# Kernel tuning notes

Measured on AMD Instinct MI355X. Metric: run time of the kernel, lower is better.

Reference implementation:

```python
import jax, jax.numpy as jnp
import numpy as np

SIGMA = 0.2
BN_EPS = 1e-5


def setup_inputs() -> dict:
    key = jax.random.key(0)
    k1, k2, k3, k4 = jax.random.split(key, 4)
    B, N, K = 8, 16384, 64
    normals = jax.random.normal(k1, (B, 3, N), dtype=jnp.float32)
    # normalize to unit normals (faithful to what the module consumes in practice)
    normals = normals / jnp.linalg.norm(normals, axis=1, keepdims=True)
    neighbor_idx = jax.random.randint(k2, (B, N, 3), 0, N, dtype=jnp.int64)
    weight_alpha = jax.random.uniform(k3, (1, K, 4), dtype=jnp.float32) * np.pi
    weight_beta = jax.random.uniform(k4, (1, K, 4), dtype=jnp.float32) * (2 * np.pi)
    bn_gamma = jnp.ones((K,), dtype=jnp.float32)
    bn_beta = jnp.zeros((K,), dtype=jnp.float32)
    return {
        "normals": normals,
        "neighbor_idx": neighbor_idx,
        "weight_alpha": weight_alpha,
        "weight_beta": weight_beta,
        "bn_gamma": bn_gamma,
        "bn_beta": bn_beta,
    }


def reference(normals, neighbor_idx, weight_alpha, weight_beta, bn_gamma, bn_beta):
    # normals: (B, 3, N); neighbor_idx: (B, N, 3)
    # kernel directions on unit sphere: W[c, k, m], c in xyz, m in 4 points per kernel
    W = jnp.concatenate(
        [
            jnp.sin(weight_alpha) * jnp.cos(weight_beta),
            jnp.sin(weight_alpha) * jnp.sin(weight_beta),
            jnp.cos(weight_alpha),
        ],
        axis=0,
    )  # (3, K, 4)

    # gather neighbor normals: nbr[b, c, i, j] = normals[b, c, neighbor_idx[b, i, j]]
    nbr = jax.vmap(lambda nm, idx: nm[:, idx])(normals, neighbor_idx)  # (B, 3, N, 3)
    F = jnp.concatenate([normals[:, :, :, None], nbr], axis=3)  # (B, 3, N, 4) face points p

    # squared distances via ||f||^2 + ||w||^2 - 2 f.w  (avoids 6D broadcast of torch code)
    dots = jnp.einsum("bcnp,ckm->bknpm", F, W)  # (B, K, N, 4, 4)
    F2 = jnp.sum(F * F, axis=1)[:, None, :, :, None]  # (B, 1, N, 4, 1)
    W2 = jnp.sum(W * W, axis=0)[None, :, None, None, :]  # (1, K, 1, 1, 4)
    dist = F2 + W2 - 2.0 * dots  # (B, K, N, 4, 4)

    inv = -1.0 / (2.0 * SIGMA * SIGMA)
    feat = jnp.sum(jnp.exp(dist * inv), axis=(3, 4)) / 16.0  # (B, K, N)

    # BatchNorm1d (training mode, biased variance over batch+spatial dims) + ReLU
    mean = jnp.mean(feat, axis=(0, 2), keepdims=True)
    var = jnp.var(feat, axis=(0, 2), keepdims=True)
    xhat = (feat - mean) * jax.lax.rsqrt(var + BN_EPS)
    out = bn_gamma[None, :, None] * xhat + bn_beta[None, :, None]
    return jax.nn.relu(out)
```

## Files before the change

### kernel.cpp

```cpp
#include <hip/hip_runtime.h>

#define BB 8
#define NN 16384
#define KK 64

#if __has_builtin(__builtin_amdgcn_exp2f)
#define EXP2(x) __builtin_amdgcn_exp2f(x)
#else
#define EXP2(x) exp2f(x)
#endif

#define LOG2E 1.44269504088896340736f
#define CW (25.0f * LOG2E)
#define CE (-12.5f * LOG2E)

__global__ __launch_bounds__(256) void fkc_main(
    const float* __restrict__ normals,
    const int*   __restrict__ nidx,
    const float* __restrict__ walpha,
    const float* __restrict__ wbeta,
    float* __restrict__ out)
{
    __shared__ float4 WV[KK * 4];

    const int tid = threadIdx.x;

    {
        float a = walpha[tid];
        float b = wbeta[tid];
        float sa = __sinf(a);
        WV[tid] = make_float4(CW * sa * __cosf(b),
                              CW * sa * __sinf(b),
                              CW * __cosf(a), 0.0f);
    }
    __syncthreads();

    const int pg = blockIdx.x >> 1;
    const int k0 = (blockIdx.x & 1) * 32;
    const int gid = pg * 256 + tid;
    const int b = gid >> 14;
    const int n = gid & (NN - 1);
    const float* nb = normals + b * 3 * NN;

    float fx[4], fy[4], fz[4], e2[4];
    fx[0] = nb[n];
    fy[0] = nb[NN + n];
    fz[0] = nb[2 * NN + n];
    const int ibase = (b * NN + n) * 3;
#pragma unroll
    for (int j = 0; j < 3; ++j) {
        int id = nidx[ibase + j];
        fx[j + 1] = nb[id];
        fy[j + 1] = nb[NN + id];
        fz[j + 1] = nb[2 * NN + id];
    }
#pragma unroll
    for (int p = 0; p < 4; ++p) {
        float n2 = fmaf(fx[p], fx[p], fmaf(fy[p], fy[p], fz[p] * fz[p]));
        e2[p] = CE * (n2 + 1.0f);
    }

    float* orow = out + (b * KK + k0) * NN + n;
#pragma unroll 2
    for (int k = 0; k < 32; ++k) {
        float acc = 0.0f;
#pragma unroll
        for (int m = 0; m < 4; ++m) {
            float4 w = WV[((k0 + k) << 2) + m];
#pragma unroll
            for (int p = 0; p < 4; ++p) {
                float arg = fmaf(fz[p], w.z,
                            fmaf(fy[p], w.y,
                            fmaf(fx[p], w.x, e2[p])));
                acc += EXP2(arg);
            }
        }
        orow[k * NN] = acc;
    }
}

__global__ __launch_bounds__(256) void fkc_reduce(
    const float4* __restrict__ out4,
    float* __restrict__ psum,
    float* __restrict__ pss)
{
    __shared__ float sw[4], ssw[4];
    const int tid = threadIdx.x;
    const int k = blockIdx.x >> 4;
    const int c = blockIdx.x & 15;
    const int b = c >> 1;
    const int half = c & 1;
    const int base4 = (b * KK + k) * (NN / 4) + half * 2048;

    float s = 0.0f, ss = 0.0f;
#pragma unroll
    for (int i = 0; i < 8; ++i) {
        float4 v = out4[base4 + tid + i * 256];
        s += v.x + v.y + v.z + v.w;
        ss += fmaf(v.x, v.x, fmaf(v.y, v.y, fmaf(v.z, v.z, v.w * v.w)));
    }
#pragma unroll
    for (int off = 1; off < 64; off <<= 1) {
        s  += __shfl_xor(s,  off, 64);
        ss += __shfl_xor(ss, off, 64);
    }
    const int wv = tid >> 6;
    if ((tid & 63) == 0) { sw[wv] = s; ssw[wv] = ss; }
    __syncthreads();
    if (tid == 0) {
        psum[blockIdx.x] = sw[0] + sw[1] + sw[2] + sw[3];
        pss[blockIdx.x]  = ssw[0] + ssw[1] + ssw[2] + ssw[3];
    }
}

__global__ __launch_bounds__(256) void fkc_apply(
    float4* __restrict__ out4,
    const float* __restrict__ psum,
    const float* __restrict__ pss,
    const float* __restrict__ gamma,
    const float* __restrict__ beta)
{
    __shared__ float s_tot, ss_tot;
    const int tid = threadIdx.x;
    const int i = blockIdx.x * 256 + tid;
    const int k = (i >> 12) & (KK - 1);

    if (tid < 32) {
        float v = (tid < 16) ? psum[k * 16 + tid] : pss[k * 16 + (tid - 16)];
#pragma unroll
        for (int off = 1; off < 16; off <<= 1) v += __shfl_xor(v, off, 64);
        if (tid == 0)  s_tot = v;
        if (tid == 16) ss_tot = v;
    }
    __syncthreads();

    const float invM = 1.0f / (float)(BB * NN);
    float mean = s_tot * invM;
    float var = fmaf(-mean, mean, ss_tot * invM);
    float sc = gamma[k] * rsqrtf(var + 1e-5f);
    float sh = fmaf(-mean, sc, beta[k]);

    float4 v = out4[i];
    v.x = fmaxf(fmaf(v.x, sc, sh), 0.0f);
    v.y = fmaxf(fmaf(v.y, sc, sh), 0.0f);
    v.z = fmaxf(fmaf(v.z, sc, sh), 0.0f);
    v.w = fmaxf(fmaf(v.w, sc, sh), 0.0f);
    out4[i] = v;
}

extern "C" void kernel_launch(void* const* d_in, const int* in_sizes, int n_in,
                              void* d_out, int out_size, void* d_ws, size_t ws_size,
                              hipStream_t stream) {
    const float* normals = (const float*)d_in[0];
    const int*   nidx    = (const int*)d_in[1];
    const float* walpha  = (const float*)d_in[2];
    const float* wbeta   = (const float*)d_in[3];
    const float* gamma   = (const float*)d_in[4];
    const float* beta    = (const float*)d_in[5];
    float* out = (float*)d_out;
    float* ws = (float*)d_ws;

    float* psum = ws;
    float* pss  = ws + 1024;

    fkc_main<<<1024, 256, 0, stream>>>(normals, nidx, walpha, wbeta, out);
    fkc_reduce<<<1024, 256, 0, stream>>>((const float4*)out, psum, pss);
    fkc_apply<<<8192, 256, 0, stream>>>((float4*)out, psum, pss, gamma, beta);
}
```

Baseline: 118.8 us.

## Fuse BN partial statistics into main kernel and precompute kernel directions

The per-channel sum and sum-of-squares are now reduced with wavefront shuffles inside the main compute kernel, which writes per-block partials. This removes the separate pass that re-read the whole output to compute statistics. Kernel directions are computed once by a tiny prep kernel and read as uniform global loads instead of being rebuilt in every block's shared memory. The main grid doubles to 16 channels per block, and a small stats kernel finalizes scale and shift so the apply kernel only does a multiply-add. The cost is one extra kernel launch plus per-channel shuffle reductions added to the main kernel.

After: 118.1 us. Within noise of the previous version (-0.6%).

```diff
diff --git a/kernel.cpp b/kernel.cpp
--- a/kernel.cpp
+++ b/kernel.cpp
@@ -3,6 +3,7 @@
 #define BB 8
 #define NN 16384
 #define KK 64
+#define NPG 512
 
 #if __has_builtin(__builtin_amdgcn_exp2f)
 #define EXP2(x) __builtin_amdgcn_exp2f(x)
@@ -14,29 +15,38 @@
 #define CW (25.0f * LOG2E)
 #define CE (-12.5f * LOG2E)
 
-__global__ __launch_bounds__(256) void fkc_main(
+__global__ __launch_bounds__(256) void fkc_prep(
+    const float* __restrict__ walpha,
+    const float* __restrict__ wbeta,
+    float* __restrict__ wx,
+    float* __restrict__ wy,
+    float* __restrict__ wz)
+{
+    const int t = threadIdx.x;
+    float a = walpha[t];
+    float b = wbeta[t];
+    float sa = __sinf(a);
+    wx[t] = CW * sa * __cosf(b);
+    wy[t] = CW * sa * __sinf(b);
+    wz[t] = CW * __cosf(a);
+}
+
+__global__ __launch_bounds__(256, 8) void fkc_main(
     const float* __restrict__ normals,
     const int*   __restrict__ nidx,
-    const float* __restrict__ walpha,
-    const float* __restrict__ wbeta,
-    float* __restrict__ out)
+    const float* __restrict__ wx,
+    const float* __restrict__ wy,
+    const float* __restrict__ wz,
+    float* __restrict__ out,
+    float* __restrict__ psum,
+    float* __restrict__ pss)
 {
-    __shared__ float4 WV[KK * 4];
+    __shared__ float reds[16][4];
+    __shared__ float redss[16][4];
 
     const int tid = threadIdx.x;
-
-    {
-        float a = walpha[tid];
-        float b = wbeta[tid];
-        float sa = __sinf(a);
-        WV[tid] = make_float4(CW * sa * __cosf(b),
-                              CW * sa * __sinf(b),
-                              CW * __cosf(a), 0.0f);
-    }
-    __syncthreads();
-
-    const int pg = blockIdx.x >> 1;
-    const int k0 = (blockIdx.x & 1) * 32;
+    const int pg = blockIdx.x >> 2;
+    const int k0 = (blockIdx.x & 3) * 16;
     const int gid = pg * 256 + tid;
     const int b = gid >> 14;
     const int n = gid & (NN - 1);
@@ -60,45 +70,60 @@
         e2[p] = CE * (n2 + 1.0f);
     }
 
+    const int lane = tid & 63;
+    const int wv = tid >> 6;
     float* orow = out + (b * KK + k0) * NN + n;
-#pragma unroll 2
-    for (int k = 0; k < 32; ++k) {
+
+#pragma unroll
+    for (int kk = 0; kk < 16; ++kk) {
         float acc = 0.0f;
 #pragma unroll
         for (int m = 0; m < 4; ++m) {
-            float4 w = WV[((k0 + k) << 2) + m];
+            const int wi = ((k0 + kk) << 2) + m;
+            float wxv = wx[wi], wyv = wy[wi], wzv = wz[wi];
 #pragma unroll
             for (int p = 0; p < 4; ++p) {
-                float arg = fmaf(fz[p], w.z,
-                            fmaf(fy[p], w.y,
-                            fmaf(fx[p], w.x, e2[p])));
+                float arg = fmaf(fz[p], wzv,
+                            fmaf(fy[p], wyv,
+                            fmaf(fx[p], wxv, e2[p])));
                 acc += EXP2(arg);
             }
         }
-        orow[k * NN] = acc;
+        orow[kk * NN] = acc;
+
+        float s = acc, ss = acc * acc;
+#pragma unroll
+        for (int off = 1; off < 64; off <<= 1) {
+            s  += __shfl_xor(s,  off, 64);
+            ss += __shfl_xor(ss, off, 64);
+        }
+        if (lane == 0) { reds[kk][wv] = s; redss[kk][wv] = ss; }
+    }
+    __syncthreads();
+
+    if (tid < 16) {
+        psum[(k0 + tid) * NPG + pg] =
+            reds[tid][0] + reds[tid][1] + reds[tid][2] + reds[tid][3];
+    } else if (tid < 32) {
+        int kk = tid - 16;
+        pss[(k0 + kk) * NPG + pg] =
+            redss[kk][0] + redss[kk][1] + redss[kk][2] + redss[kk][3];
     }
 }
 
-__global__ __launch_bounds__(256) void fkc_reduce(
-    const float4* __restrict__ out4,
-    float* __restrict__ psum,
-    float* __restrict__ pss)
+__global__ __launch_bounds__(256) void fkc_stats(
+    const float* __restrict__ psum,
+    const float* __restrict__ pss,
+    const float* __restrict__ gamma,
+    const float* __restrict__ beta,
+    float* __restrict__ fin)
 {
     __shared__ float sw[4], ssw[4];
     const int tid = threadIdx.x;
-    const int k = blockIdx.x >> 4;
-    const int c = blockIdx.x & 15;
-    const int b = c >> 1;
-    const int half = c & 1;
-    const int base4 = (b * KK + k) * (NN / 4) + half * 2048;
+    const int k = blockIdx.x;
 
-    float s = 0.0f, ss = 0.0f;
-#pragma unroll
-    for (int i = 0; i < 8; ++i) {
-        float4 v = out4[base4 + tid + i * 256];
-        s += v.x + v.y + v.z + v.w;
-        ss += fmaf(v.x, v.x, fmaf(v.y, v.y, fmaf(v.z, v.z, v.w * v.w)));
-    }
+    float s  = psum[k * NPG + tid] + psum[k * NPG + 256 + tid];
+    float ss = pss[k * NPG + tid]  + pss[k * NPG + 256 + tid];
 #pragma unroll
     for (int off = 1; off < 64; off <<= 1) {
         s  += __shfl_xor(s,  off, 64);
@@ -108,38 +133,25 @@
     if ((tid & 63) == 0) { sw[wv] = s; ssw[wv] = ss; }
     __syncthreads();
     if (tid == 0) {
-        psum[blockIdx.x] = sw[0] + sw[1] + sw[2] + sw[3];
-        pss[blockIdx.x]  = ssw[0] + ssw[1] + ssw[2] + ssw[3];
+        float st  = sw[0] + sw[1] + sw[2] + sw[3];
+        float sst = ssw[0] + ssw[1] + ssw[2] + ssw[3];
+        const float invM = 1.0f / (float)(BB * NN);
+        float mean = st * invM;
+        float var = fmaf(-mean, mean, sst * invM);
+        float sc = gamma[k] * rsqrtf(var + 1e-5f);
+        fin[k] = sc;
+        fin[KK + k] = fmaf(-mean, sc, beta[k]);
     }
 }
 
 __global__ __launch_bounds__(256) void fkc_apply(
     float4* __restrict__ out4,
-    const float* __restrict__ psum,
-    const float* __restrict__ pss,
-    const float* __restrict__ gamma,
-    const float* __restrict__ beta)
+    const float* __restrict__ fin)
 {
-    __shared__ float s_tot, ss_tot;
-    const int tid = threadIdx.x;
-    const int i = blockIdx.x * 256 + tid;
+    const int i = blockIdx.x * 256 + threadIdx.x;
     const int k = (i >> 12) & (KK - 1);
-
-    if (tid < 32) {
-        float v = (tid < 16) ? psum[k * 16 + tid] : pss[k * 16 + (tid - 16)];
-#pragma unroll
-        for (int off = 1; off < 16; off <<= 1) v += __shfl_xor(v, off, 64);
-        if (tid == 0)  s_tot = v;
-        if (tid == 16) ss_tot = v;
-    }
-    __syncthreads();
-
-    const float invM = 1.0f / (float)(BB * NN);
-    float mean = s_tot * invM;
-    float var = fmaf(-mean, mean, ss_tot * invM);
-    float sc = gamma[k] * rsqrtf(var + 1e-5f);
-    float sh = fmaf(-mean, sc, beta[k]);
-
+    const float sc = fin[k];
+    const float sh = fin[KK + k];
     float4 v = out4[i];
     v.x = fmaxf(fmaf(v.x, sc, sh), 0.0f);
     v.y = fmaxf(fmaf(v.y, sc, sh), 0.0f);
@@ -161,9 +173,15 @@
     float* ws = (float*)d_ws;
 
     float* psum = ws;
-    float* pss  = ws + 1024;
+    float* pss  = ws + KK * NPG;
+    float* fin  = ws + 2 * KK * NPG;
+    float* wxb  = ws + 2 * KK * NPG + 128;
+    float* wyb  = wxb + 256;
+    float* wzb  = wyb + 256;
 
-    fkc_main<<<1024, 256, 0, stream>>>(normals, nidx, walpha, wbeta, out);
-    fkc_reduce<<<1024, 256, 0, stream>>>((const float4*)out, psum, pss);
-    fkc_apply<<<8192, 256, 0, stream>>>((float4*)out, psum, pss, gamma, beta);
+    fkc_prep<<<1, 256, 0, stream>>>(walpha, wbeta, wxb, wyb, wzb);
+    fkc_main<<<2048, 256, 0, stream>>>(normals, nidx, wxb, wyb, wzb,
+                                       out, psum, pss);
+    fkc_stats<<<KK, 256, 0, stream>>>(psum, pss, gamma, beta, fin);
+    fkc_apply<<<8192, 256, 0, stream>>>((float4*)out, fin);
 }
```
